# Kernel optimization log

Measured on AMD Instinct MI355X. Metric: run time of the kernel, lower is better.

The kernel has to match this reference:

```python
import jax, jax.numpy as jnp
import numpy as np

N = 16384          # num nodes
D_IN, D_HID, D_OUT = 512, 256, 64
S = 4096           # sampled nodes per layer


def setup_inputs() -> dict:
    key = jax.random.key(0)
    ks = jax.random.split(key, 8)
    X = jax.random.normal(ks[0], (N, D_IN), dtype=jnp.float32)
    A_hat = jax.random.uniform(ks[1], (N, N), dtype=jnp.float32)
    W1 = jax.random.normal(ks[2], (D_IN, D_HID), dtype=jnp.float32) * 0.05
    b1 = jax.random.normal(ks[3], (D_HID,), dtype=jnp.float32) * 0.05
    W2 = jax.random.normal(ks[4], (D_HID, D_OUT), dtype=jnp.float32) * 0.05
    b2 = jax.random.normal(ks[5], (D_OUT,), dtype=jnp.float32) * 0.05
    # unique sampled node ids per layer (avoids nondeterministic duplicate scatter)
    sampled_l0 = jax.random.permutation(ks[6], N)[:S].astype(jnp.int32)
    sampled_l1 = jax.random.permutation(ks[7], N)[:S].astype(jnp.int32)
    return {"X": X, "A_hat": A_hat, "W1": W1, "b1": b1, "W2": W2, "b2": b2,
            "sampled_l0": sampled_l0, "sampled_l1": sampled_l1}


def reference(X, A_hat, W1, b1, W2, b2, sampled_l0, sampled_l1):
    n = X.shape[0]
    s0 = sampled_l0.shape[0]
    s1 = sampled_l1.shape[0]

    # ---- layer 0: sampled = l0, next_sampled = l1 ----
    H_l = jax.nn.relu(X[sampled_l0] @ W1 + b1)                 # [S, D_HID]
    # weights[i,j] = A_hat[next[i], sampled[j]] * N / S  (sampling_probs=None path)
    w0 = A_hat[sampled_l1][:, sampled_l0] * (n / s0)           # [S, S]
    agg0 = w0 @ H_l                                            # [S, D_HID]
    H = jnp.zeros((n, W1.shape[1]), dtype=X.dtype).at[sampled_l1].set(agg0)
    H = jax.nn.relu(H)                                         # inter-layer relu

    # ---- layer 1 (last): sampled = l1, next_sampled = arange(N) ----
    H_l2 = jax.nn.relu(H[sampled_l1] @ W2 + b2)                # [S, D_OUT]
    w1 = A_hat[:, sampled_l1] * (n / s1)                       # [N, S]
    out = w1 @ H_l2                                            # [N, D_OUT]; scatter to arange(N) == identity
    return out
```

## Files before the change

### kernel.cpp

```cpp
#include <hip/hip_runtime.h>
#include <hip/hip_bf16.h>
#include <stdint.h>

typedef __attribute__((ext_vector_type(8))) short short8;
typedef __attribute__((ext_vector_type(4))) float f32x4;

#define N_NODES 16384
#define D_IN    512
#define D_HID   256
#define D_OUT   64
#define S_SAMP  4096

__device__ __forceinline__ unsigned short f2bf(float f) {
  __hip_bfloat16 h = __float2bfloat16(f);
  union { __hip_bfloat16 h; unsigned short u; } cv; cv.h = h; return cv.u;
}

template<int BM, int BN, int BK, bool RELU_A, int MINW>
__global__ __launch_bounds__(256, MINW)
void gemm_tn(const float* __restrict__ A, int lda,
             const int* __restrict__ arow,
             const unsigned short* __restrict__ Bt, int ldb,
             float* __restrict__ C, int ldc,
             int K, int kChunks, float scale)
{
  static_assert(BM == 64 && (BK == 32 || BK == 64) && (BN == 64 || BN == 256), "tile");
  constexpr int CH    = BK / 8;
  constexpr int RPS   = 512 / BK;
  constexpr int SLABS = BN / RPS;
  constexpr int SLABW = SLABS / 4;
  constexpr int AV    = BK / 16;
  constexpr int AC    = BK / 32;

  const int mt  = blockIdx.x / kChunks;
  const int kc  = blockIdx.x % kChunks;
  const int kLen = K / kChunks;
  const int k0   = kc * kLen;
  const int nt   = kLen / BK;
  const int tid  = threadIdx.x;
  const int lane = tid & 63;
  const int wid  = tid >> 6;
  const int l16  = lane & 15;
  const int lg   = lane >> 4;

  __shared__ unsigned short As[2][BM * BK];
  __shared__ unsigned short Bs[2][BN * BK];

  constexpr int WN  = (BN == 256) ? 4 : 2;
  constexpr int WM  = 4 / WN;
  constexpr int WTM = BM / WM;
  constexpr int WTN = BN / WN;
  constexpr int MF  = WTM / 16;
  constexpr int NF  = WTN / 16;
  const int wrow = wid / WN;
  const int wcol = wid % WN;

  f32x4 acc[MF][NF] = {};

  const int am   = tid >> 2;
  const int aseg = tid & 3;
  const int arowIdx = mt * BM + am;
  const size_t rowg = arow ? (size_t)arow[arowIdx] : (size_t)arowIdx;
  const float* aBase = A + rowg * (size_t)lda + k0 + aseg * (BK / 4);

  const int brow = lane / CH;
  const int bcol = 8 * ((lane % CH) ^ (brow & (CH - 1)));
  const unsigned short* bSrc = Bt + (size_t)brow * ldb + k0 + bcol;

  f32x4 av[AV];

  auto loadA = [&](int ks) {
    #pragma unroll
    for (int i = 0; i < AV; ++i) av[i] = *(const f32x4*)(aBase + ks + 4 * i);
  };
  auto writeA = [&](int buf) {
    if (RELU_A) {
      #pragma unroll
      for (int i = 0; i < AV; ++i)
        #pragma unroll
        for (int j = 0; j < 4; ++j) av[i][j] = fmaxf(av[i][j], 0.f);
    }
    #pragma unroll
    for (int c = 0; c < AC; ++c) {
      short8 s;
      s[0]=f2bf(av[2*c][0]);   s[1]=f2bf(av[2*c][1]);
      s[2]=f2bf(av[2*c][2]);   s[3]=f2bf(av[2*c][3]);
      s[4]=f2bf(av[2*c+1][0]); s[5]=f2bf(av[2*c+1][1]);
      s[6]=f2bf(av[2*c+1][2]); s[7]=f2bf(av[2*c+1][3]);
      const int g = (aseg * AC + c) ^ (am & (CH - 1));
      *(short8*)&As[buf][am * BK + g * 8] = s;
    }
  };
  auto issueB = [&](int buf, int ks) {
    #pragma unroll
    for (int i = 0; i < SLABW; ++i) {
      const int s = wid * SLABW + i;
      __builtin_amdgcn_global_load_lds(
          (const __attribute__((address_space(1))) uint32_t*)(bSrc + (size_t)s * RPS * ldb + ks),
          (__attribute__((address_space(3))) uint32_t*)(&Bs[buf][s * 512]),
          16, 0, 0);
    }
  };
  auto compute = [&](int buf) {
    #pragma unroll
    for (int kk = 0; kk < BK / 32; ++kk) {
      const int gk = kk * 4 + lg;
      short8 af[MF], bfr[NF];
      #pragma unroll
      for (int fm = 0; fm < MF; ++fm) {
        const int m = wrow * WTM + fm * 16 + l16;
        af[fm] = *(const short8*)&As[buf][m * BK + ((gk ^ (m & (CH - 1))) * 8)];
      }
      #pragma unroll
      for (int fn = 0; fn < NF; ++fn) {
        const int n = wcol * WTN + fn * 16 + l16;
        bfr[fn] = *(const short8*)&Bs[buf][n * BK + ((gk ^ (n & (CH - 1))) * 8)];
      }
      #pragma unroll
      for (int fm = 0; fm < MF; ++fm)
        #pragma unroll
        for (int fn = 0; fn < NF; ++fn)
          acc[fm][fn] = __builtin_amdgcn_mfma_f32_16x16x32_bf16(
              af[fm], bfr[fn], acc[fm][fn], 0, 0, 0);
    }
  };

  loadA(0);
  issueB(0, 0);
  writeA(0);
  __syncthreads();

  int cur = 0;
  for (int t = 0; t < nt; ++t) {
    const bool more = (t + 1 < nt);
    if (more) {
      loadA((t + 1) * BK);
      issueB(cur ^ 1, (t + 1) * BK);
    }
    compute(cur);
    if (more) writeA(cur ^ 1);
    __syncthreads();
    cur ^= 1;
  }

  #pragma unroll
  for (int fm = 0; fm < MF; ++fm)
    #pragma unroll
    for (int fn = 0; fn < NF; ++fn)
      #pragma unroll
      for (int j = 0; j < 4; ++j) {
        const int r = mt * BM + wrow * WTM + fm * 16 + lg * 4 + j;
        const int c = wcol * WTN + fn * 16 + l16;
        atomicAdd(&C[(size_t)r * ldc + c], scale * acc[fm][fn][j]);
      }
}

__global__ void conv_w_t(const float* __restrict__ W1, const float* __restrict__ W2,
                         unsigned short* __restrict__ W1t, unsigned short* __restrict__ W2t) {
  const int idx = blockIdx.x * 256 + threadIdx.x;
  if (idx < D_IN * D_HID) {
    const int j = idx / D_IN, i = idx % D_IN;
    W1t[idx] = f2bf(W1[(size_t)i * D_HID + j]);
  }
  if (idx < D_HID * D_OUT) {
    const int j = idx / D_HID, i = idx % D_HID;
    W2t[idx] = f2bf(W2[(size_t)i * D_OUT + j]);
  }
}

__global__ void ep_scatter_t(const float* __restrict__ G, const float* __restrict__ bias,
                             const int* __restrict__ rows, unsigned short* __restrict__ BextT,
                             int ncol, int total) {
  const int idx = blockIdx.x * 256 + threadIdx.x;
  if (idx >= total) return;
  const int c = idx / S_SAMP;
  const int r = idx & (S_SAMP - 1);
  float v = G[(size_t)r * ncol + c] + bias[c];
  v = v > 0.f ? v : 0.f;
  BextT[(size_t)c * N_NODES + rows[r]] = f2bf(v);
}

extern "C" void kernel_launch(void* const* d_in, const int* in_sizes, int n_in,
                              void* d_out, int out_size, void* d_ws, size_t ws_size,
                              hipStream_t stream) {
  const float* X     = (const float*)d_in[0];
  const float* A_hat = (const float*)d_in[1];
  const float* W1    = (const float*)d_in[2];
  const float* b1    = (const float*)d_in[3];
  const float* W2    = (const float*)d_in[4];
  const float* b2    = (const float*)d_in[5];
  const int*   l0    = (const int*)d_in[6];
  const int*   l1    = (const int*)d_in[7];
  float* out = (float*)d_out;

  if (ws_size < (size_t)(20u << 20)) return;
  char* ws = (char*)d_ws;
  unsigned short* HextT = (unsigned short*)(ws);
  unsigned short* PextT = (unsigned short*)(ws + (8  << 20));
  float* G1 = (float*)(ws + (10 << 20));
  float* G2 = (float*)(ws + (14 << 20));
  float* G3 = (float*)(ws + (18 << 20));
  unsigned short* W1t = (unsigned short*)(ws + (19 << 20));
  unsigned short* W2t = (unsigned short*)(ws + (19 << 20) + (256 << 10));

  hipMemsetAsync(ws,  0, (size_t)(19u << 20), stream);
  hipMemsetAsync(out, 0, (size_t)N_NODES * D_OUT * 4, stream);

  conv_w_t<<<512, 256, 0, stream>>>(W1, W2, W1t, W2t);

  gemm_tn<64, 256, 32, false, 4><<<(S_SAMP / 64) * 8, 256, 0, stream>>>(
      X, D_IN, l0, W1t, D_IN, G1, D_HID, D_IN, 8, 1.0f);
  ep_scatter_t<<<(S_SAMP * D_HID + 255) / 256, 256, 0, stream>>>(
      G1, b1, l0, HextT, D_HID, S_SAMP * D_HID);

  gemm_tn<64, 256, 32, false, 4><<<(S_SAMP / 64) * 16, 256, 0, stream>>>(
      A_hat, N_NODES, l1, HextT, N_NODES, G2, D_HID, N_NODES, 16, 4.0f);

  gemm_tn<64, 64, 32, true, 8><<<(S_SAMP / 64) * 4, 256, 0, stream>>>(
      G2, D_HID, nullptr, W2t, D_HID, G3, D_OUT, D_HID, 4, 1.0f);
  ep_scatter_t<<<(S_SAMP * D_OUT + 255) / 256, 256, 0, stream>>>(
      G3, b2, l1, PextT, D_OUT, S_SAMP * D_OUT);

  gemm_tn<64, 64, 32, false, 8><<<(N_NODES / 64) * 8, 256, 0, stream>>>(
      A_hat, N_NODES, nullptr, PextT, N_NODES, out, D_OUT, N_NODES, 8, 4.0f);
}
```

Baseline: 430.9 us.

## Load A operand directly into MFMA register fragments, bypassing LDS staging

Adds a gemm_direct kernel in which each wave loads its 16 rows of fp32 A straight from global memory into registers in MFMA fragment layout. It converts them to bf16 in registers, so A no longer goes through an LDS write and read. Only B is staged through double-buffered LDS via global_load_lds, and the loop is unrolled two tiles at a time with ping-pong register buffers for A. The two large A_hat GEMMs now use this kernel, aiming to cut LDS traffic and synchronisation on the bandwidth-bound A_hat reads. In exchange, every wave must read the full B tile from LDS, the loop assumes an even tile count, and occupancy settings change.

```diff
diff --git a/kernel.cpp b/kernel.cpp
--- a/kernel.cpp
+++ b/kernel.cpp
@@ -14,6 +14,101 @@
 __device__ __forceinline__ unsigned short f2bf(float f) {
   __hip_bfloat16 h = __float2bfloat16(f);
   union { __hip_bfloat16 h; unsigned short u; } cv; cv.h = h; return cv.u;
+}
+
+template<int BN, int BK, int MINW>
+__global__ __launch_bounds__(256, MINW)
+void gemm_direct(const float* __restrict__ A, int lda,
+                 const int* __restrict__ arow,
+                 const unsigned short* __restrict__ Bt, int ldb,
+                 float* __restrict__ C, int ldc,
+                 int K, int kChunks, float scale)
+{
+  constexpr int NF    = BN / 16;
+  constexpr int KKS   = BK / 32;
+  constexpr int CH    = BK / 8;
+  constexpr int RPS   = 512 / BK;
+  constexpr int SLABS = BN / RPS;
+  constexpr int SLABW = SLABS / 4;
+
+  const int mt   = blockIdx.x / kChunks;
+  const int kc   = blockIdx.x % kChunks;
+  const int kLen = K / kChunks;
+  const int k0   = kc * kLen;
+  const int nt   = kLen / BK;
+  const int tid  = threadIdx.x;
+  const int lane = tid & 63;
+  const int wid  = tid >> 6;
+  const int l16  = lane & 15;
+  const int lg   = lane >> 4;
+
+  __shared__ unsigned short Bs[2][BN * BK];
+
+  const int r = mt * 64 + wid * 16 + l16;
+  const size_t ra = arow ? (size_t)arow[r] : (size_t)r;
+  const float* aPtr = A + ra * (size_t)lda + k0 + lg * 8;
+
+  const int brow = lane / CH;
+  const int bcol = 8 * ((lane % CH) ^ (brow & (CH - 1)));
+  const unsigned short* bSrc = Bt + (size_t)brow * ldb + k0 + bcol;
+
+  f32x4 acc[NF] = {};
+  f32x4 avA[2 * KKS], avB[2 * KKS];
+
+  auto issueB = [&](int buf, int t) {
+    #pragma unroll
+    for (int i = 0; i < SLABW; ++i) {
+      const int s = wid * SLABW + i;
+      __builtin_amdgcn_global_load_lds(
+          (const __attribute__((address_space(1))) uint32_t*)(bSrc + (size_t)s * RPS * ldb + t * BK),
+          (__attribute__((address_space(3))) uint32_t*)(&Bs[buf][s * 512]),
+          16, 0, 0);
+    }
+  };
+  auto loadA = [&](f32x4 (&av)[2 * KKS], int t) {
+    #pragma unroll
+    for (int kk = 0; kk < KKS; ++kk) {
+      av[2 * kk]     = *(const f32x4*)(aPtr + t * BK + kk * 32);
+      av[2 * kk + 1] = *(const f32x4*)(aPtr + t * BK + kk * 32 + 4);
+    }
+  };
+  auto compute = [&](int buf, f32x4 (&av)[2 * KKS]) {
+    #pragma unroll
+    for (int kk = 0; kk < KKS; ++kk) {
+      short8 af;
+      af[0] = f2bf(av[2*kk][0]);   af[1] = f2bf(av[2*kk][1]);
+      af[2] = f2bf(av[2*kk][2]);   af[3] = f2bf(av[2*kk][3]);
+      af[4] = f2bf(av[2*kk+1][0]); af[5] = f2bf(av[2*kk+1][1]);
+      af[6] = f2bf(av[2*kk+1][2]); af[7] = f2bf(av[2*kk+1][3]);
+      #pragma unroll
+      for (int fn = 0; fn < NF; ++fn) {
+        const int n = fn * 16 + l16;
+        short8 b = *(const short8*)&Bs[buf][n * BK + (((kk * 4 + lg) ^ (n & (CH - 1))) * 8)];
+        acc[fn] = __builtin_amdgcn_mfma_f32_16x16x32_bf16(af, b, acc[fn], 0, 0, 0);
+      }
+    }
+  };
+
+  loadA(avA, 0);
+  issueB(0, 0);
+
+  for (int t = 0; t + 2 <= nt; t += 2) {
+    __syncthreads();
+    if (t + 1 < nt) { issueB(1, t + 1); loadA(avB, t + 1); }
+    compute(0, avA);
+    __syncthreads();
+    if (t + 2 < nt) { issueB(0, t + 2); loadA(avA, t + 2); }
+    compute(1, avB);
+  }
+
+  #pragma unroll
+  for (int fn = 0; fn < NF; ++fn)
+    #pragma unroll
+    for (int j = 0; j < 4; ++j) {
+      const int rr = mt * 64 + wid * 16 + lg * 4 + j;
+      const int cc = fn * 16 + l16;
+      atomicAdd(&C[(size_t)rr * ldc + cc], scale * acc[fn][j]);
+    }
 }
 
 template<int BM, int BN, int BK, bool RELU_A, int MINW>
@@ -149,9 +244,9 @@
     for (int fn = 0; fn < NF; ++fn)
       #pragma unroll
       for (int j = 0; j < 4; ++j) {
-        const int r = mt * BM + wrow * WTM + fm * 16 + lg * 4 + j;
-        const int c = wcol * WTN + fn * 16 + l16;
-        atomicAdd(&C[(size_t)r * ldc + c], scale * acc[fm][fn][j]);
+        const int rr = mt * BM + wrow * WTM + fm * 16 + lg * 4 + j;
+        const int cc = wcol * WTN + fn * 16 + l16;
+        atomicAdd(&C[(size_t)rr * ldc + cc], scale * acc[fm][fn][j]);
       }
 }
 
@@ -213,7 +308,7 @@
   ep_scatter_t<<<(S_SAMP * D_HID + 255) / 256, 256, 0, stream>>>(
       G1, b1, l0, HextT, D_HID, S_SAMP * D_HID);
 
-  gemm_tn<64, 256, 32, false, 4><<<(S_SAMP / 64) * 16, 256, 0, stream>>>(
+  gemm_direct<256, 32, 4><<<(S_SAMP / 64) * 16, 256, 0, stream>>>(
       A_hat, N_NODES, l1, HextT, N_NODES, G2, D_HID, N_NODES, 16, 4.0f);
 
   gemm_tn<64, 64, 32, true, 8><<<(S_SAMP / 64) * 4, 256, 0, stream>>>(
@@ -221,6 +316,6 @@
   ep_scatter_t<<<(S_SAMP * D_OUT + 255) / 256, 256, 0, stream>>>(
       G3, b2, l1, PextT, D_OUT, S_SAMP * D_OUT);
 
-  gemm_tn<64, 64, 32, false, 8><<<(N_NODES / 64) * 8, 256, 0, stream>>>(
+  gemm_direct<64, 64, 6><<<(N_NODES / 64) * 8, 256, 0, stream>>>(
       A_hat, N_NODES, nullptr, PextT, N_NODES, out, D_OUT, N_NODES, 8, 4.0f);
 }
```

Result: no change. 423.6 us (-1.7%).
